# Kernel tuning notes

Measured on AMD Instinct MI355X. Metric: run time of the kernel, lower is better.

The kernel has to match this reference:

```python
import jax, jax.numpy as jnp
import numpy as np

D_MODEL = 1024
N_HEADS = 16
HEAD_DIM = D_MODEL // N_HEADS


def setup_inputs() -> dict:
    key = jax.random.key(0)
    ks = jax.random.split(key, 9)
    s = 0.02
    x = jax.random.normal(ks[0], (2, 2048, D_MODEL), dtype=jnp.float32)
    wq = jax.random.normal(ks[1], (D_MODEL, D_MODEL), dtype=jnp.float32) * s
    wk = jax.random.normal(ks[2], (D_MODEL, D_MODEL), dtype=jnp.float32) * s
    wv = jax.random.normal(ks[3], (D_MODEL, D_MODEL), dtype=jnp.float32) * s
    wo = jax.random.normal(ks[4], (D_MODEL, D_MODEL), dtype=jnp.float32) * s
    bq = jax.random.normal(ks[5], (D_MODEL,), dtype=jnp.float32) * s
    bk = jax.random.normal(ks[6], (D_MODEL,), dtype=jnp.float32) * s
    bv = jax.random.normal(ks[7], (D_MODEL,), dtype=jnp.float32) * s
    bo = jax.random.normal(ks[8], (D_MODEL,), dtype=jnp.float32) * s
    return {"x": x, "wq": wq, "bq": bq, "wk": wk, "bk": bk,
            "wv": wv, "bv": bv, "wo": wo, "bo": bo}


def reference(x, wq, bq, wk, bk, wv, bv, wo, bo):
    B, T, C = x.shape
    H, Dh = N_HEADS, HEAD_DIM
    # torch Linear: y = x @ W.T + b
    q = (x @ wq.T + bq).reshape(B, T, H, Dh).transpose(0, 2, 1, 3)  # [B,H,T,Dh]
    k = (x @ wk.T + bk).reshape(B, T, H, Dh).transpose(0, 2, 1, 3)
    v = (x @ wv.T + bv).reshape(B, T, H, Dh).transpose(0, 2, 1, 3)
    scale = 1.0 / jnp.sqrt(jnp.float32(Dh))
    score = jnp.einsum('bhqd,bhkd->bhqk', q, k) * scale  # [B,H,T,T]
    causal = jnp.triu(jnp.ones((T, T), dtype=jnp.bool_), k=1)
    score = jnp.where(causal[None, None], jnp.float32(-10000.0), score)
    attn = jax.nn.softmax(score, axis=-1)
    out = jnp.einsum('bhqk,bhkd->bhqd', attn, v)  # [B,H,T,Dh]
    out = out.transpose(0, 2, 1, 3).reshape(B, T, C)
    return out @ wo.T + bo
```

## Files before the change

kernel.cpp:

```cpp
#include <hip/hip_runtime.h>
#include <hip/hip_bf16.h>

typedef __bf16 bf16_t;
typedef __bf16 bf16x8 __attribute__((ext_vector_type(8)));
typedef __bf16 bf16x4 __attribute__((ext_vector_type(4)));
typedef float f32x4 __attribute__((ext_vector_type(4)));
typedef unsigned int u32;

#define D_MODEL 1024
#define T_SEQ   2048
#define N_HEADS 16

#define WAITVM(N) asm volatile("s_waitcnt vmcnt(" #N ")" ::: "memory")

__device__ __forceinline__ void gload_lds16(const void* g, void* l) {
  __builtin_amdgcn_global_load_lds((const __attribute__((address_space(1))) u32*)g,
                                   (__attribute__((address_space(3))) u32*)l, 16, 0, 0);
}

__device__ __forceinline__ float fast_exp2(float x) {
#if __has_builtin(__builtin_amdgcn_exp2f)
  return __builtin_amdgcn_exp2f(x);
#else
  return __expf(x * 0.69314718056f);
#endif
}

struct CastArgs { const float* src[5]; bf16_t* dst[5]; };

__global__ __launch_bounds__(256) void cast_all(CastArgs p) {
  unsigned i = (blockIdx.x * 256u + threadIdx.x) * 4u;
  int seg; unsigned off;
  if (i < 4194304u) { seg = 0; off = i; }
  else { unsigned r = i - 4194304u; seg = 1 + (int)(r >> 20); off = r & 1048575u; }
  const float4 v = *(const float4*)(p.src[seg] + off);
  bf16x4 o = { (bf16_t)v.x, (bf16_t)v.y, (bf16_t)v.z, (bf16_t)v.w };
  *(bf16x4*)(p.dst[seg] + off) = o;
}

#define QSCL 0.18033688011112042f

struct QKVArgs {
  const bf16_t* A;
  const bf16_t* W[3];
  const float* bias[3];
  bf16_t* out[3];
};

__global__ __launch_bounds__(512, 2) void qkv_gemm(QKVArgs p) {
  __shared__ bf16_t lds[2 * 28672];

  const int tid = threadIdx.x;
  const int l = tid & 63, wid = tid >> 6;
  const int lh = l >> 4, r15 = l & 15;

  const int lid = blockIdx.x;
  const int bx = lid >> 4, by = lid & 15;
  const int brow = bx * 256;
  const int gcol0 = by * 192;

  const int wr = (wid >> 2) * 128;
  const int wc = (wid & 3) * 48;
  const int wrc = (wr >> 4);
  const int wcc = (wc >> 4);
  const int sA = (lh ^ ((r15 >> 1) & 3)) * 8;
  const int roff = r15 * 32;

  const int srow = l >> 2;
  const int gs = ((l & 3) ^ ((l >> 3) & 3)) * 8;

  f32x4 acc[8][3];
  const f32x4 zero = {0.f, 0.f, 0.f, 0.f};
#pragma unroll
  for (int i = 0; i < 8; ++i)
#pragma unroll
    for (int j = 0; j < 3; ++j) acc[i][j] = zero;

  const bf16_t* A = p.A;

  auto stageA = [&](bf16_t* buf, int k0, int kh) {
#pragma unroll
    for (int i = 0; i < 2; ++i) {
      int c = wid * 2 + i;
      gload_lds16(A + (size_t)(brow + c * 16 + srow) * D_MODEL + k0 + kh * 32 + gs,
                  buf + kh * 8192 + c * 512);
    }
  };
  auto stageB = [&](bf16_t* buf, int k0) {
#pragma unroll
    for (int i = 0; i < 3; ++i) {
      int g = wid * 3 + i;
      int kh = g >= 12;
      int c = g - kh * 12;
      int gcol = gcol0 + c * 16 + srow;
      int z = gcol >> 10;
      const bf16_t* w = (z == 0) ? p.W[0] : ((z == 1) ? p.W[1] : p.W[2]);
      gload_lds16(w + (size_t)(gcol & 1023) * D_MODEL + k0 + kh * 32 + gs,
                  buf + 16384 + kh * 6144 + c * 512);
    }
  };

  stageA(lds, 0, 0);
  stageA(lds, 0, 1);
  stageB(lds, 0);
  WAITVM(0);
  __builtin_amdgcn_s_barrier();

  for (int t = 0; t < 16; ++t) {
    bf16_t* cur = lds + (t & 1) * 28672;
    bf16_t* nxt = lds + ((t + 1) & 1) * 28672;
    const int k1 = (t + 1) * 64;
    const bool more = (t < 15);

    bf16x8 bfr[3][2];
#pragma unroll
    for (int ph = 0; ph < 4; ++ph) {
      bf16x8 a[2][2];
#pragma unroll
      for (int jj = 0; jj < 2; ++jj)
#pragma unroll
        for (int kh = 0; kh < 2; ++kh)
          a[jj][kh] = *(const bf16x8*)(cur + kh * 8192 + (wrc + 2 * ph + jj) * 512 + roff + sA);
      if (ph == 0) {
#pragma unroll
        for (int ni = 0; ni < 3; ++ni)
#pragma unroll
          for (int kh = 0; kh < 2; ++kh)
            bfr[ni][kh] = *(const bf16x8*)(cur + 16384 + kh * 6144 + (wcc + ni) * 512 + roff + sA);
      }
      if (more) {
        if (ph == 0) stageA(nxt, k1, 0);
        else if (ph == 1) stageA(nxt, k1, 1);
        else if (ph == 2) stageB(nxt, k1);
      }
      __builtin_amdgcn_s_barrier();
      __builtin_amdgcn_s_setprio(1);
#pragma unroll
      for (int jj = 0; jj < 2; ++jj)
#pragma unroll
        for (int ni = 0; ni < 3; ++ni) {
          acc[2 * ph + jj][ni] = __builtin_amdgcn_mfma_f32_16x16x32_bf16(a[jj][0], bfr[ni][0], acc[2 * ph + jj][ni], 0, 0, 0);
          acc[2 * ph + jj][ni] = __builtin_amdgcn_mfma_f32_16x16x32_bf16(a[jj][1], bfr[ni][1], acc[2 * ph + jj][ni], 0, 0, 0);
        }
      __builtin_amdgcn_s_setprio(0);
      if (ph == 3 && more) WAITVM(0);
      __builtin_amdgcn_s_barrier();
    }
  }

#pragma unroll
  for (int ni = 0; ni < 3; ++ni) {
    const int col = gcol0 + wc + ni * 16 + r15;
    const int z = col >> 10;
    const int zc = col & 1023;
    const float* bias = (z == 0) ? p.bias[0] : ((z == 1) ? p.bias[1] : p.bias[2]);
    bf16_t* O = (z == 0) ? p.out[0] : ((z == 1) ? p.out[1] : p.out[2]);
    const float bz = bias[zc];
    if (z == 2) {
#pragma unroll
      for (int mi = 0; mi < 8; ++mi) {
        int row0 = brow + wr + mi * 16 + lh * 4;
        int bb = row0 >> 11, t0 = row0 & 2047;
        bf16x4 pk;
#pragma unroll
        for (int j = 0; j < 4; ++j) pk[j] = (bf16_t)(acc[mi][ni][j] + bz);
        *(bf16x4*)(O + (size_t)bb * (D_MODEL * T_SEQ) + (size_t)zc * T_SEQ + t0) = pk;
      }
    } else if (z == 0) {
#pragma unroll
      for (int mi = 0; mi < 8; ++mi) {
        int row0 = brow + wr + mi * 16 + lh * 4;
#pragma unroll
        for (int j = 0; j < 4; ++j)
          O[(size_t)(row0 + j) * D_MODEL + zc] = (bf16_t)((acc[mi][ni][j] + bz) * QSCL);
      }
    } else {
#pragma unroll
      for (int mi = 0; mi < 8; ++mi) {
        int row0 = brow + wr + mi * 16 + lh * 4;
#pragma unroll
        for (int j = 0; j < 4; ++j)
          O[(size_t)(row0 + j) * D_MODEL + zc] = (bf16_t)(acc[mi][ni][j] + bz);
      }
    }
  }
}

__device__ __forceinline__ void stage_ab64(
    const bf16_t* __restrict__ A, const bf16_t* __restrict__ W,
    bf16_t* buf, int brow, int bcol, int k0, int w, int l) {
  const int srow = l >> 2;
  const int scol = ((l & 3) ^ ((l >> 3) & 3)) * 8;
#pragma unroll
  for (int i = 0; i < 3; ++i) {
    int ch = w * 3 + i;
    const bf16_t* src = (ch < 4)
      ? A + (size_t)(brow + ch * 16 + srow) * D_MODEL + k0 + scol
      : W + (size_t)(bcol + (ch - 4) * 16 + srow) * D_MODEL + k0 + scol;
    gload_lds16(src, buf + ch * 512);
  }
}

__device__ __forceinline__ void gemm_tile_64(
    const bf16_t* __restrict__ A, const bf16_t* __restrict__ W,
    bf16_t* bufs, int brow, int bcol, f32x4 acc[2][4])
{
  const int tid = threadIdx.x;
  const int l = tid & 63, w = tid >> 6;
  const int wr = (w >> 1) * 32, wc = (w & 1) * 64;
  const int lh = l >> 4, r15 = l & 15;
  const int NS = D_MODEL / 32;

  stage_ab64(A, W, bufs + 0 * 6144, brow, bcol, 0, w, l);
  stage_ab64(A, W, bufs + 1 * 6144, brow, bcol, 32, w, l);

  for (int t = 0; t < NS; ++t) {
    bf16_t* bb = bufs + (t % 3) * 6144;
    if (t + 2 < NS) {
      stage_ab64(A, W, bufs + ((t + 2) % 3) * 6144, brow, bcol, (t + 2) * 32, w, l);
      WAITVM(6);
    } else if (t + 1 < NS) {
      WAITVM(3);
    } else {
      WAITVM(0);
    }
    __builtin_amdgcn_s_barrier();

    bf16x8 af[2], bfr[4];
#pragma unroll
    for (int mi = 0; mi < 2; ++mi) {
      int rr = wr + mi * 16 + r15;
      int s = lh ^ ((rr >> 1) & 3);
      af[mi] = *(const bf16x8*)(bb + rr * 32 + s * 8);
    }
#pragma unroll
    for (int ni = 0; ni < 4; ++ni) {
      int rr = wc + ni * 16 + r15;
      int s = lh ^ ((rr >> 1) & 3);
      bfr[ni] = *(const bf16x8*)(bb + 2048 + rr * 32 + s * 8);
    }
    __builtin_amdgcn_s_setprio(1);
#pragma unroll
    for (int mi = 0; mi < 2; ++mi)
#pragma unroll
      for (int ni = 0; ni < 4; ++ni)
        acc[mi][ni] = __builtin_amdgcn_mfma_f32_16x16x32_bf16(af[mi], bfr[ni], acc[mi][ni], 0, 0, 0);
    __builtin_amdgcn_s_setprio(0);
    __builtin_amdgcn_s_barrier();
  }
}

__global__ __launch_bounds__(256) void out_gemm(
    const bf16_t* __restrict__ A, const bf16_t* __restrict__ W,
    const float* __restrict__ bias, float* __restrict__ O)
{
  __shared__ bf16_t bufs[3 * 6144];
  f32x4 acc[2][4];
  f32x4 zero = {0.f, 0.f, 0.f, 0.f};
#pragma unroll
  for (int i = 0; i < 2; ++i)
#pragma unroll
    for (int j = 0; j < 4; ++j) acc[i][j] = zero;

  const int brow = blockIdx.x * 64, bcol = blockIdx.y * 128;
  gemm_tile_64(A, W, bufs, brow, bcol, acc);

  const int tid = threadIdx.x, l = tid & 63, w = tid >> 6;
  const int wr = (w >> 1) * 32, wc = (w & 1) * 64, lh = l >> 4, r15 = l & 15;
#pragma unroll
  for (int ni = 0; ni < 4; ++ni) {
    int col = bcol + wc + ni * 16 + r15;
    float bz = bias[col];
#pragma unroll
    for (int mi = 0; mi < 2; ++mi) {
      int row0 = brow + wr + mi * 16 + lh * 4;
#pragma unroll
      for (int j = 0; j < 4; ++j)
        O[(size_t)(row0 + j) * D_MODEL + col] = acc[mi][ni][j] + bz;
    }
  }
}

__device__ __forceinline__ void stage_kv128(const bf16_t* Kg, const bf16_t* Vg,
                                            bf16_t* Kd, bf16_t* Vd, int kv0, int w, int l) {
#pragma unroll
  for (int i = 0; i < 4; ++i) {
    int c = w * 4 + i;
    int row = c * 8 + (l >> 3);
    int gcol = ((l & 7) ^ ((l >> 3) & 7)) * 8;
    gload_lds16(Kg + (size_t)(kv0 + row) * D_MODEL + gcol, Kd + c * 512);
  }
#pragma unroll
  for (int i = 0; i < 4; ++i) {
    int c = w * 4 + i;
    int drow = c * 4 + (l >> 4);
    int gkv = ((l & 15) ^ (drow & 15)) * 8;
    gload_lds16(Vg + (size_t)drow * T_SEQ + kv0 + gkv, Vd + c * 512);
  }
}

__global__ __launch_bounds__(256) void flash_attn(
    const bf16_t* __restrict__ Qm, const bf16_t* __restrict__ Km,
    const bf16_t* __restrict__ Vtg, bf16_t* __restrict__ Om)
{
  __shared__ bf16_t Kls[2][128 * 64];
  __shared__ bf16_t Vls[2][64 * 128];
  __shared__ bf16_t Pls[4][16 * 72];

  const int tid = threadIdx.x, l = tid & 63, w = tid >> 6;
  const int lh = l >> 4, r15 = l & 15;

  const int lid = blockIdx.x;
  const int xcd = lid & 7;
  const int idx = lid >> 3;
  const int pair = idx & 15;
  const int bh = xcd + 8 * (idx >> 4);
  const int b = bh >> 4, h = bh & 15;
  const int qtA = pair, qtB = 31 - pair;
  const int nA = (qtA >> 1) + 1;
  const int NT = 17;

  const size_t baseQ = (size_t)b * T_SEQ * D_MODEL + h * 64;
  const size_t baseVt = (size_t)b * (D_MODEL * T_SEQ) + (size_t)(h * 64) * T_SEQ;
  const bf16_t* Kg = Km + baseQ;
  const bf16_t* Vg = Vtg + baseVt;

  int qw = qtA * 64 + w * 16;

  bf16x8 qf[2];
  {
    const bf16_t* qp = Qm + baseQ + (size_t)(qw + r15) * D_MODEL + lh * 8;
    qf[0] = *(const bf16x8*)(qp);
    qf[1] = *(const bf16x8*)(qp + 32);
  }

  float l_r = 0.f;
  f32x4 o_acc[4];
  const f32x4 zero = {0.f, 0.f, 0.f, 0.f};
#pragma unroll
  for (int n = 0; n < 4; ++n) o_acc[n] = zero;

  bf16_t* P = &Pls[w][0];

  stage_kv128(Kg, Vg, Kls[0], Vls[0], 0, w, l);

  for (int t = 0; t < NT; ++t) {
    const int buf = t & 1;
    if (t + 1 < NT) {
      const int nt = t + 1;
      const int nkv0 = (nt < nA) ? nt * 128 : (nt - nA) * 128;
      stage_kv128(Kg, Vg, Kls[buf ^ 1], Vls[buf ^ 1], nkv0, w, l);
      WAITVM(8);
    } else {
      WAITVM(0);
    }
    __builtin_amdgcn_s_barrier();

    const int kv0 = (t < nA) ? t * 128 : (t - nA) * 128;
    const int qt_cur = (t < nA) ? qtA : qtB;
    const bool diag = (t == nA - 1) || (t == NT - 1);
    const bool skip2 = diag && ((qt_cur & 1) == 0);
    const bf16_t* Kb = Kls[buf];
    const bf16_t* Vb = Vls[buf];
    const int qrow = qw + r15;

    f32x4 sf[8];
    auto qk_n = [&](int n) {
      const int kvc = n * 16 + r15;
      const int sw = kvc & 7;
      bf16x8 kf0 = *(const bf16x8*)(Kb + kvc * 64 + ((lh ^ sw) * 8));
      bf16x8 kf1 = *(const bf16x8*)(Kb + kvc * 64 + (((4 + lh) ^ sw) * 8));
      f32x4 a = zero;
      a = __builtin_amdgcn_mfma_f32_16x16x32_bf16(kf0, qf[0], a, 0, 0, 0);
      a = __builtin_amdgcn_mfma_f32_16x16x32_bf16(kf1, qf[1], a, 0, 0, 0);
      sf[n] = a;
    };
    auto sm_half = [&](int hh, bool dm) {
#pragma unroll
      for (int n2 = 0; n2 < 4; ++n2) {
        const int n = hh * 4 + n2;
        float pv[4];
#pragma unroll
        for (int j = 0; j < 4; ++j) {
          float pp = fast_exp2(sf[n][j]);
          if (dm) {
            const int kvcol = kv0 + hh * 64 + n2 * 16 + lh * 4 + j;
            if (kvcol > qrow) pp = 0.f;
          }
          pv[j] = pp;
          l_r += pp;
        }
        bf16x4 pk = { (bf16_t)pv[0], (bf16_t)pv[1], (bf16_t)pv[2], (bf16_t)pv[3] };
        *(bf16x4*)(P + r15 * 72 + (n2 * 2 + (lh >> 1)) * 8 + (lh & 1) * 4) = pk;
      }
    };
    auto pv_half = [&](int hh) {
      bf16x8 pa0 = *(const bf16x8*)(P + r15 * 72 + lh * 8);
      bf16x8 pa1 = *(const bf16x8*)(P + r15 * 72 + (4 + lh) * 8);
      __builtin_amdgcn_s_setprio(1);
#pragma unroll
      for (int nD = 0; nD < 4; ++nD) {
        const int d = nD * 16 + r15;
        const int b0 = (hh * 8 + lh) ^ r15;
        const int b1 = (hh * 8 + 4 + lh) ^ r15;
        bf16x8 vf0 = *(const bf16x8*)(Vb + d * 128 + b0 * 8);
        bf16x8 vf1 = *(const bf16x8*)(Vb + d * 128 + b1 * 8);
        o_acc[nD] = __builtin_amdgcn_mfma_f32_16x16x32_bf16(vf0, pa0, o_acc[nD], 0, 0, 0);
        o_acc[nD] = __builtin_amdgcn_mfma_f32_16x16x32_bf16(vf1, pa1, o_acc[nD], 0, 0, 0);
      }
      __builtin_amdgcn_s_setprio(0);
    };

    __builtin_amdgcn_s_setprio(1);
#pragma unroll
    for (int n = 0; n < 4; ++n) qk_n(n);
    __builtin_amdgcn_s_setprio(0);
    if (!skip2) {
      __builtin_amdgcn_s_setprio(1);
#pragma unroll
      for (int n = 4; n < 8; ++n) qk_n(n);
      __builtin_amdgcn_s_setprio(0);
    }

    if (diag) {
      sm_half(0, true);
      pv_half(0);
      if (!skip2) { sm_half(1, true); pv_half(1); }
    } else {
      sm_half(0, false);
      pv_half(0);
      sm_half(1, false);
      pv_half(1);
    }

    __builtin_amdgcn_s_barrier();

    if (t == nA - 1) {
      float ls = l_r;
      ls += __shfl_xor(ls, 16, 64);
      ls += __shfl_xor(ls, 32, 64);
      const float invl = 1.f / ls;
      bf16_t* orow = Om + (size_t)(b * T_SEQ + qw + r15) * D_MODEL + h * 64;
#pragma unroll
      for (int n = 0; n < 4; ++n) {
        bf16x4 pk = { (bf16_t)(o_acc[n][0] * invl), (bf16_t)(o_acc[n][1] * invl),
                      (bf16_t)(o_acc[n][2] * invl), (bf16_t)(o_acc[n][3] * invl) };
        *(bf16x4*)(orow + n * 16 + lh * 4) = pk;
      }
      qw = qtB * 64 + w * 16;
      const bf16_t* qp = Qm + baseQ + (size_t)(qw + r15) * D_MODEL + lh * 8;
      qf[0] = *(const bf16x8*)(qp);
      qf[1] = *(const bf16x8*)(qp + 32);
      l_r = 0.f;
#pragma unroll
      for (int n = 0; n < 4; ++n) o_acc[n] = zero;
    }
  }

  float ls = l_r;
  ls += __shfl_xor(ls, 16, 64);
  ls += __shfl_xor(ls, 32, 64);
  const float invl = 1.f / ls;
  bf16_t* orow = Om + (size_t)(b * T_SEQ + qw + r15) * D_MODEL + h * 64;
#pragma unroll
  for (int n = 0; n < 4; ++n) {
    bf16x4 pk = { (bf16_t)(o_acc[n][0] * invl), (bf16_t)(o_acc[n][1] * invl),
                  (bf16_t)(o_acc[n][2] * invl), (bf16_t)(o_acc[n][3] * invl) };
    *(bf16x4*)(orow + n * 16 + lh * 4) = pk;
  }
}

extern "C" void kernel_launch(void* const* d_in, const int* in_sizes, int n_in,
                              void* d_out, int out_size, void* d_ws, size_t ws_size,
                              hipStream_t stream) {
  const float* x  = (const float*)d_in[0];
  const float* wq = (const float*)d_in[1];
  const float* bq = (const float*)d_in[2];
  const float* wk = (const float*)d_in[3];
  const float* bk = (const float*)d_in[4];
  const float* wv = (const float*)d_in[5];
  const float* bv = (const float*)d_in[6];
  const float* wo = (const float*)d_in[7];
  const float* bo = (const float*)d_in[8];

  char* ws = (char*)d_ws;
  const size_t MB = 1024 * 1024;
  bf16_t* xb  = (bf16_t*)(ws);
  bf16_t* wqb = (bf16_t*)(ws + 8 * MB);
  bf16_t* wkb = (bf16_t*)(ws + 10 * MB);
  bf16_t* wvb = (bf16_t*)(ws + 12 * MB);
  bf16_t* wob = (bf16_t*)(ws + 14 * MB);
  bf16_t* qb  = (bf16_t*)(ws + 16 * MB);
  bf16_t* kb  = (bf16_t*)(ws + 24 * MB);
  bf16_t* vtb = (bf16_t*)(ws + 32 * MB);
  bf16_t* ob  = (bf16_t*)(ws + 40 * MB);

  CastArgs ca;
  ca.src[0] = x;  ca.dst[0] = xb;
  ca.src[1] = wq; ca.dst[1] = wqb;
  ca.src[2] = wk; ca.dst[2] = wkb;
  ca.src[3] = wv; ca.dst[3] = wvb;
  ca.src[4] = wo; ca.dst[4] = wob;
  cast_all<<<8192, 256, 0, stream>>>(ca);

  QKVArgs qa;
  qa.A = xb;
  qa.W[0] = wqb; qa.W[1] = wkb; qa.W[2] = wvb;
  qa.bias[0] = bq; qa.bias[1] = bk; qa.bias[2] = bv;
  qa.out[0] = qb; qa.out[1] = kb; qa.out[2] = vtb;
  qkv_gemm<<<256, 512, 0, stream>>>(qa);

  flash_attn<<<512, 256, 0, stream>>>(qb, kb, vtb, ob);

  out_gemm<<<dim3(64, 8), 256, 0, stream>>>(ob, wob, bo, (float*)d_out);
}
```

Measured before the change: 97.38 us.

## Single-buffer K/V with staggered prefetch and one query tile per block

```diff
diff --git a/kernel.cpp b/kernel.cpp
--- a/kernel.cpp
+++ b/kernel.cpp
@@ -281,8 +281,7 @@
   }
 }
 
-__device__ __forceinline__ void stage_kv128(const bf16_t* Kg, const bf16_t* Vg,
-                                            bf16_t* Kd, bf16_t* Vd, int kv0, int w, int l) {
+__device__ __forceinline__ void stage_k128(const bf16_t* Kg, bf16_t* Kd, int kv0, int w, int l) {
 #pragma unroll
   for (int i = 0; i < 4; ++i) {
     int c = w * 4 + i;
@@ -290,6 +289,8 @@
     int gcol = ((l & 7) ^ ((l >> 3) & 7)) * 8;
     gload_lds16(Kg + (size_t)(kv0 + row) * D_MODEL + gcol, Kd + c * 512);
   }
+}
+__device__ __forceinline__ void stage_v128(const bf16_t* Vg, bf16_t* Vd, int kv0, int w, int l) {
 #pragma unroll
   for (int i = 0; i < 4; ++i) {
     int c = w * 4 + i;
@@ -303,29 +304,26 @@
     const bf16_t* __restrict__ Qm, const bf16_t* __restrict__ Km,
     const bf16_t* __restrict__ Vtg, bf16_t* __restrict__ Om)
 {
-  __shared__ bf16_t Kls[2][128 * 64];
-  __shared__ bf16_t Vls[2][64 * 128];
-  __shared__ bf16_t Pls[4][16 * 72];
+  __shared__ bf16_t Kls[128 * 64];
+  __shared__ bf16_t Vls[64 * 128];
+  __shared__ bf16_t Pls[4][2][16 * 72];
 
   const int tid = threadIdx.x, l = tid & 63, w = tid >> 6;
   const int lh = l >> 4, r15 = l & 15;
 
   const int lid = blockIdx.x;
-  const int xcd = lid & 7;
-  const int idx = lid >> 3;
-  const int pair = idx & 15;
-  const int bh = xcd + 8 * (idx >> 4);
+  const int qt = 31 - (lid >> 5);
+  const int bh = lid & 31;
   const int b = bh >> 4, h = bh & 15;
-  const int qtA = pair, qtB = 31 - pair;
-  const int nA = (qtA >> 1) + 1;
-  const int NT = 17;
+  const int nT = (qt >> 1) + 1;
 
   const size_t baseQ = (size_t)b * T_SEQ * D_MODEL + h * 64;
   const size_t baseVt = (size_t)b * (D_MODEL * T_SEQ) + (size_t)(h * 64) * T_SEQ;
   const bf16_t* Kg = Km + baseQ;
   const bf16_t* Vg = Vtg + baseVt;
 
-  int qw = qtA * 64 + w * 16;
+  const int qw = qt * 64 + w * 16;
+  const int qrow = qw + r15;
 
   bf16x8 qf[2];
   {
@@ -340,42 +338,46 @@
 #pragma unroll
   for (int n = 0; n < 4; ++n) o_acc[n] = zero;
 
-  bf16_t* P = &Pls[w][0];
-
-  stage_kv128(Kg, Vg, Kls[0], Vls[0], 0, w, l);
-
-  for (int t = 0; t < NT; ++t) {
-    const int buf = t & 1;
-    if (t + 1 < NT) {
-      const int nt = t + 1;
-      const int nkv0 = (nt < nA) ? nt * 128 : (nt - nA) * 128;
-      stage_kv128(Kg, Vg, Kls[buf ^ 1], Vls[buf ^ 1], nkv0, w, l);
-      WAITVM(8);
-    } else {
-      WAITVM(0);
-    }
-    __builtin_amdgcn_s_barrier();
-
-    const int kv0 = (t < nA) ? t * 128 : (t - nA) * 128;
-    const int qt_cur = (t < nA) ? qtA : qtB;
-    const bool diag = (t == nA - 1) || (t == NT - 1);
-    const bool skip2 = diag && ((qt_cur & 1) == 0);
-    const bf16_t* Kb = Kls[buf];
-    const bf16_t* Vb = Vls[buf];
-    const int qrow = qw + r15;
+  bf16_t* PA = &Pls[w][0][0];
+  bf16_t* PB = &Pls[w][1][0];
+
+  stage_k128(Kg, Kls, 0, w, l);
+  stage_v128(Vg, Vls, 0, w, l);
+  WAITVM(0);
+  __builtin_amdgcn_s_barrier();
+
+  for (int t = 0; t < nT; ++t) {
+    const int kv0 = t * 128;
+    const bool more = (t + 1 < nT);
+    const bool diag = (t == nT - 1);
+    const bool skip2 = diag && ((qt & 1) == 0);
 
     f32x4 sf[8];
     auto qk_n = [&](int n) {
       const int kvc = n * 16 + r15;
       const int sw = kvc & 7;
-      bf16x8 kf0 = *(const bf16x8*)(Kb + kvc * 64 + ((lh ^ sw) * 8));
-      bf16x8 kf1 = *(const bf16x8*)(Kb + kvc * 64 + (((4 + lh) ^ sw) * 8));
+      bf16x8 kf0 = *(const bf16x8*)(Kls + kvc * 64 + ((lh ^ sw) * 8));
+      bf16x8 kf1 = *(const bf16x8*)(Kls + kvc * 64 + (((4 + lh) ^ sw) * 8));
       f32x4 a = zero;
       a = __builtin_amdgcn_mfma_f32_16x16x32_bf16(kf0, qf[0], a, 0, 0, 0);
       a = __builtin_amdgcn_mfma_f32_16x16x32_bf16(kf1, qf[1], a, 0, 0, 0);
       sf[n] = a;
     };
-    auto sm_half = [&](int hh, bool dm) {
+    __builtin_amdgcn_s_setprio(1);
+#pragma unroll
+    for (int n = 0; n < 4; ++n) qk_n(n);
+    __builtin_amdgcn_s_setprio(0);
+    if (!skip2) {
+      __builtin_amdgcn_s_setprio(1);
+#pragma unroll
+      for (int n = 4; n < 8; ++n) qk_n(n);
+      __builtin_amdgcn_s_setprio(0);
+    }
+
+    __builtin_amdgcn_s_barrier();
+    if (more) stage_k128(Kg, Kls, kv0 + 128, w, l);
+
+    auto sm_half = [&](int hh, bf16_t* P, bool dm) {
 #pragma unroll
       for (int n2 = 0; n2 < 4; ++n2) {
         const int n = hh * 4 + n2;
@@ -394,7 +396,12 @@
         *(bf16x4*)(P + r15 * 72 + (n2 * 2 + (lh >> 1)) * 8 + (lh & 1) * 4) = pk;
       }
     };
-    auto pv_half = [&](int hh) {
+    sm_half(0, PA, diag);
+    if (!skip2) sm_half(1, PB, diag);
+
+    if (more) WAITVM(4); else WAITVM(0);
+
+    auto pv_half = [&](int hh, const bf16_t* P) {
       bf16x8 pa0 = *(const bf16x8*)(P + r15 * 72 + lh * 8);
       bf16x8 pa1 = *(const bf16x8*)(P + r15 * 72 + (4 + lh) * 8);
       __builtin_amdgcn_s_setprio(1);
@@ -403,57 +410,20 @@
         const int d = nD * 16 + r15;
         const int b0 = (hh * 8 + lh) ^ r15;
         const int b1 = (hh * 8 + 4 + lh) ^ r15;
-        bf16x8 vf0 = *(const bf16x8*)(Vb + d * 128 + b0 * 8);
-        bf16x8 vf1 = *(const bf16x8*)(Vb + d * 128 + b1 * 8);
+        bf16x8 vf0 = *(const bf16x8*)(Vls + d * 128 + b0 * 8);
+        bf16x8 vf1 = *(const bf16x8*)(Vls + d * 128 + b1 * 8);
         o_acc[nD] = __builtin_amdgcn_mfma_f32_16x16x32_bf16(vf0, pa0, o_acc[nD], 0, 0, 0);
         o_acc[nD] = __builtin_amdgcn_mfma_f32_16x16x32_bf16(vf1, pa1, o_acc[nD], 0, 0, 0);
       }
       __builtin_amdgcn_s_setprio(0);
     };
-
-    __builtin_amdgcn_s_setprio(1);
-#pragma unroll
-    for (int n = 0; n < 4; ++n) qk_n(n);
-    __builtin_amdgcn_s_setprio(0);
-    if (!skip2) {
-      __builtin_amdgcn_s_setprio(1);
-#pragma unroll
-      for (int n = 4; n < 8; ++n) qk_n(n);
-      __builtin_amdgcn_s_setprio(0);
-    }
-
-    if (diag) {
-      sm_half(0, true);
-      pv_half(0);
-      if (!skip2) { sm_half(1, true); pv_half(1); }
-    } else {
-      sm_half(0, false);
-      pv_half(0);
-      sm_half(1, false);
-      pv_half(1);
-    }
+    pv_half(0, PA);
+    if (!skip2) pv_half(1, PB);
 
     __builtin_amdgcn_s_barrier();
-
-    if (t == nA - 1) {
-      float ls = l_r;
-      ls += __shfl_xor(ls, 16, 64);
-      ls += __shfl_xor(ls, 32, 64);
-      const float invl = 1.f / ls;
-      bf16_t* orow = Om + (size_t)(b * T_SEQ + qw + r15) * D_MODEL + h * 64;
-#pragma unroll
-      for (int n = 0; n < 4; ++n) {
-        bf16x4 pk = { (bf16_t)(o_acc[n][0] * invl), (bf16_t)(o_acc[n][1] * invl),
-                      (bf16_t)(o_acc[n][2] * invl), (bf16_t)(o_acc[n][3] * invl) };
-        *(bf16x4*)(orow + n * 16 + lh * 4) = pk;
-      }
-      qw = qtB * 64 + w * 16;
-      const bf16_t* qp = Qm + baseQ + (size_t)(qw + r15) * D_MODEL + lh * 8;
-      qf[0] = *(const bf16x8*)(qp);
-      qf[1] = *(const bf16x8*)(qp + 32);
-      l_r = 0.f;
-#pragma unroll
-      for (int n = 0; n < 4; ++n) o_acc[n] = zero;
+    if (more) {
+      stage_v128(Vg, Vls, kv0 + 128, w, l);
+      WAITVM(4);
     }
   }
 
@@ -510,7 +480,7 @@
   qa.out[0] = qb; qa.out[1] = kb; qa.out[2] = vtb;
   qkv_gemm<<<256, 512, 0, stream>>>(qa);
 
-  flash_attn<<<512, 256, 0, stream>>>(qb, kb, vtb, ob);
+  flash_attn<<<1024, 256, 0, stream>>>(qb, kb, vtb, ob);
 
   out_gemm<<<dim3(64, 8), 256, 0, stream>>>(ob, wob, bo, (float*)d_out);
 }
```

New measurement: 94.70 us. -2.8%, faster.
